# Kernel optimization log

Measured on AMD Instinct MI355X. Metric: run time of the kernel, lower is better.

Reference implementation:

```python
import jax, jax.numpy as jnp
import numpy as np

EPS = 1e-6  # VN-ReLU direction-norm epsilon
K_NN = 16


def vec_linear(x, W):
    # x: (B, Cin, 3, ...), W: (Cout, Cin) -> (B, Cout, 3, ...)
    return jnp.einsum('oi,bi...->bo...', W, x)


def vec_lna(x, W, U):
    # VecLinear + VN-LeakyReLU(negative_slope=0) acting on vector dim (axis 2)
    p = jnp.einsum('oi,bi...->bo...', W, x)   # feature map
    d = jnp.einsum('oi,bi...->bo...', U, x)   # direction map
    dot = jnp.sum(p * d, axis=2, keepdims=True)
    dsq = jnp.sum(d * d, axis=2, keepdims=True)
    return jnp.where(dot >= 0, p, p - (dot / (dsq + EPS)) * d)


def setup_inputs() -> dict:
    B, N = 2, 4096
    h, c, L = 128, 128, 4
    ks = jax.random.split(jax.random.key(0), 8)
    s = lambda k, shape, fan: (jax.random.normal(k, shape, jnp.float32) / np.sqrt(fan)).astype(jnp.float32)
    return {
        'x': jax.random.normal(ks[0], (B, 3, N), jnp.float32),
        'W_in': s(ks[1], (h, 3), 3),
        'U_in': s(ks[2], (h, 3), 3),
        'Wl': s(ks[3], (L, h, h), h),
        'Ul': s(ks[4], (L, h, h), h),
        'Wg': s(ks[5], (L, h, 2 * h), 2 * h),
        'Ug': s(ks[6], (L, h, 2 * h), 2 * h),
        'W_out': s(ks[7], (c, L * h), L * h),
    }


def reference(x, W_in, U_in, Wl, Ul, Wg, Ug, W_out):
    B, _, N = x.shape
    K = K_NN
    pts = jnp.transpose(x, (0, 2, 1))                      # (B, N, 3)
    # squared euclidean distance (same KNN ordering as torch.cdist p=2 + topk smallest)
    sq = jnp.sum(pts * pts, axis=-1)                       # (B, N)
    d2 = sq[:, :, None] + sq[:, None, :] - 2.0 * jnp.einsum('bnd,bmd->bnm', pts, pts)
    _, idx = jax.lax.top_k(-d2, K)                         # (B, N, K) nearest, sorted
    neighbors = jax.vmap(lambda p, i: p[i])(pts, idx)      # (B, N, K, 3) gather
    neighbors = jnp.transpose(neighbors, (0, 3, 1, 2))[:, None]  # (B, 1, 3, N, K)

    x4 = x[:, None]                                        # (B, 1, 3, N)
    x_pad = jnp.broadcast_to(x4[..., None], neighbors.shape)
    # F.normalize(x, dim=2) with eps=1e-12 clamp
    x_dir = x4 / jnp.maximum(jnp.linalg.norm(x4, axis=2, keepdims=True), 1e-12)
    cross = jnp.cross(jnp.broadcast_to(x_dir[..., None], neighbors.shape), neighbors, axis=2)
    y = jnp.concatenate([cross, neighbors - x_pad, x_pad], axis=1)  # (B, 3, 3, N, K)

    h_feat = vec_lna(y, W_in, U_in)                        # (B, h, 3, N, K)
    h_feat = jnp.mean(h_feat, axis=-1)                     # meanpool over K -> (B, h, 3, N)

    y = h_feat
    feats = []
    for i in range(Wl.shape[0]):
        y = vec_lna(y, Wl[i], Ul[i])                       # (B, h, 3, N)
        yg = jnp.mean(y, axis=-1, keepdims=True)
        y = jnp.concatenate([y, jnp.broadcast_to(yg, y.shape)], axis=1)  # (B, 2h, 3, N)
        y = vec_lna(y, Wg[i], Ug[i])                       # (B, h, 3, N)
        feats.append(y)

    out = vec_linear(jnp.concatenate(feats, axis=1), W_out)  # (B, c, 3, N)
    return (jnp.mean(out, axis=-1), out)
```

## Files before the change

### kernel.cpp

```cpp
#include <hip/hip_runtime.h>
#include <hip/hip_bf16.h>
#include <cfloat>


typedef __attribute__((ext_vector_type(8))) short short8;
typedef __attribute__((ext_vector_type(4))) float f32x4;

__device__ __forceinline__ unsigned short f2bf(float f) {
    union { float f; unsigned u; } v; v.f = f;
    unsigned r = v.u + 0x7fffu + ((v.u >> 16) & 1u);
    return (unsigned short)(r >> 16);
}
__device__ __forceinline__ float bf2f(unsigned short h) {
    union { unsigned u; float f; } v; v.u = ((unsigned)h) << 16;
    return v.f;
}

__global__ __launch_bounds__(256) void setup_kernel(const float* __restrict__ x,
                                                    float4* __restrict__ pts4,
                                                    const float* __restrict__ Wl,
                                                    const float* __restrict__ Ul,
                                                    const float* __restrict__ Wg,
                                                    const float* __restrict__ Ug,
                                                    const float* __restrict__ Wout,
                                                    unsigned short* __restrict__ Ah,
                                                    unsigned short* __restrict__ Al,
                                                    int N, int B) {
    int t = blockIdx.x * 256 + threadIdx.x;
    if (t < B * N) {
        int b = t / N, n = t - b * N;
        const float* xb = x + (long)b * 3 * N;
        float px = xb[n], py = xb[N + n], pz = xb[2 * N + n];
        pts4[t] = make_float4(px, py, pz, px * px + py * py + pz * pz);
    }
    int g, r, M; long base;
    if (t < 262144) { g = t >> 15; r = t & 32767; M = 256; base = (long)g << 15; }
    else { int t2 = t - 262144; g = 8 + (t2 >> 14); r = t2 & 16383; M = 128;
           base = 262144 + (long)(g - 8) * 16384; }
    int MF = M >> 4;
    int ks = r / (MF * 512);
    int mf = (r >> 9) % MF;
    int lane = (r >> 3) & 63;
    int j = r & 7;
    int m = mf * 16 + (lane & 15);
    int k = ks * 32 + ((lane >> 4) << 3) + j;
    const float* src; int ldw; int row;
    if (g < 4) {
        ldw = 128; row = m & 127;
        src = (m < 128) ? (Wl + (long)g * 128 * 128) : (Ul + (long)g * 128 * 128);
    } else if (g < 8) {
        ldw = 256; row = m & 127;
        int l = g - 4;
        src = (m < 128) ? (Wg + (long)l * 128 * 256) : (Ug + (long)l * 128 * 256);
    } else {
        ldw = 512; row = m;
        src = Wout + (g - 8) * 128;
    }
    float v = src[(long)row * ldw + k];
    unsigned short h = f2bf(v);
    Ah[base + r] = h;
    Al[base + r] = f2bf(v - bf2f(h));
}

__global__ __launch_bounds__(1024) void knn_kernel(const float4* __restrict__ pts4,
                                                   int* __restrict__ idxOut, int N) {
    __shared__ float4 cbuf[4096];
    int t = threadIdx.x;
    int tilesPerB = N / 16;
    int b = blockIdx.x / tilesPerB;
    int q = (blockIdx.x % tilesPerB) * 16 + (t >> 6);
    int lane = t & 63;

    for (int i = t; i < N; i += 1024) cbuf[i] = pts4[b * N + i];
    __syncthreads();

    float4 Q = cbuf[q];
    unsigned ku; int ki;

    {
        float4 C = cbuf[lane];
        float dot = Q.x * C.x + Q.y * C.y + Q.z * C.z;
        float d2 = Q.w + C.w - 2.0f * dot;
        unsigned u = __float_as_uint(d2);
        u ^= (unsigned)((int)u >> 31) | 0x80000000u;
        double key = (double)u * 4096.0 + (double)lane;
#pragma unroll
        for (int k = 2; k <= 64; k <<= 1) {
#pragma unroll
            for (int j = k >> 1; j > 0; j >>= 1) {
                double other = __shfl_xor(key, j);
                bool takeMin = (((lane & j) == 0) == ((lane & k) == 0));
                double mn = fmin(key, other), mx = fmax(key, other);
                key = takeMin ? mn : mx;
            }
        }
        long long kl = (long long)key;
        ki = (int)(kl & 4095);
        ku = (unsigned)(kl >> 12);
    }
    unsigned Tu = (unsigned)__builtin_amdgcn_readlane((int)ku, 15);

    for (int c0 = 64; c0 < N; c0 += 64) {
        float4 C = cbuf[c0 + lane];
        float dot = Q.x * C.x + Q.y * C.y + Q.z * C.z;
        float d2 = Q.w + C.w - 2.0f * dot;
        unsigned u = __float_as_uint(d2);
        u ^= (unsigned)((int)u >> 31) | 0x80000000u;
        int ci = c0 + lane;
        unsigned long long mask = __ballot(u <= Tu);
        while (mask) {
            int src = __ffsll(mask) - 1;
            mask &= mask - 1;
            unsigned vu = (unsigned)__builtin_amdgcn_readlane((int)u, src);
            int      vi = __builtin_amdgcn_readlane(ci, src);
            unsigned kum1 = (unsigned)__builtin_amdgcn_update_dpp(
                                (int)ku, (int)ku, 0x111, 0xF, 0xF, false);
            int      kim1 = __builtin_amdgcn_update_dpp(
                                ki, ki, 0x111, 0xF, 0xF, false);
            if (lane == 0) { kum1 = 0u; kim1 = (-2147483647 - 1); }
            bool lem1 = (vu < kum1) || (vu == kum1 && vi < kim1);
            bool ltj  = (vu < ku)   || (vu == ku   && vi < ki);
            unsigned knu = lem1 ? kum1 : (ltj ? vu : ku);
            int      kni = lem1 ? kim1 : (ltj ? vi : ki);
            if (lane < 16) { ku = knu; ki = kni; }
        }
        Tu = (unsigned)__builtin_amdgcn_readlane((int)ku, 15);
    }
    if (lane < 16) idxOut[(b * N + q) * 16 + lane] = ki;
}

__global__ __launch_bounds__(256) void edge_kernel(const float4* __restrict__ pts4,
                                                   const int* __restrict__ idx,
                                                   const float* __restrict__ Win,
                                                   const float* __restrict__ Uin,
                                                   unsigned short* __restrict__ Yh,
                                                   unsigned short* __restrict__ Yl,
                                                   int N) {
    __shared__ float4 nbuf[8][16];
    __shared__ float4 cpt[8];
    int nTiles = N / 8;
    int b = blockIdx.x / nTiles;
    int n0 = (blockIdx.x % nTiles) * 8;
    int t = threadIdx.x;
    if (t < 128) {
        int pl = t >> 4, k = t & 15;
        int nb = idx[(b * N + n0 + pl) * 16 + k];
        nbuf[pl][k] = pts4[b * N + nb];
    } else if (t < 136) {
        cpt[t - 128] = pts4[b * N + n0 + (t - 128)];
    }
    __syncthreads();
    int o = t & 127, h = t >> 7;
    float w0 = Win[o * 3], w1 = Win[o * 3 + 1], w2 = Win[o * 3 + 2];
    float u0 = Uin[o * 3], u1 = Uin[o * 3 + 1], u2 = Uin[o * 3 + 2];
    for (int pl = h * 4; pl < h * 4 + 4; ++pl) {
        float4 c4 = cpt[pl];
        float inv = 1.0f / fmaxf(sqrtf(c4.w), 1e-12f);
        float ax = c4.x * inv, ay = c4.y * inv, az = c4.z * inv;
        float a0 = 0.f, a1 = 0.f, a2 = 0.f;
        for (int k = 0; k < 16; ++k) {
            float4 nb = nbuf[pl][k];
            float cr0 = ay * nb.z - az * nb.y;
            float cr1 = az * nb.x - ax * nb.z;
            float cr2 = ax * nb.y - ay * nb.x;
            float df0 = nb.x - c4.x, df1 = nb.y - c4.y, df2 = nb.z - c4.z;
            float P0 = w0 * cr0 + w1 * df0 + w2 * c4.x;
            float P1 = w0 * cr1 + w1 * df1 + w2 * c4.y;
            float P2 = w0 * cr2 + w1 * df2 + w2 * c4.z;
            float D0 = u0 * cr0 + u1 * df0 + u2 * c4.x;
            float D1 = u0 * cr1 + u1 * df1 + u2 * c4.y;
            float D2 = u0 * cr2 + u1 * df2 + u2 * c4.z;
            float dot = P0 * D0 + P1 * D1 + P2 * D2;
            float dsq = D0 * D0 + D1 * D1 + D2 * D2;
            if (dot < 0.0f) {
                float s = dot / (dsq + 1e-6f);
                P0 -= s * D0; P1 -= s * D1; P2 -= s * D2;
            }
            a0 += P0; a1 += P1; a2 += P2;
        }
        float vals[3] = { a0 * (1.0f / 16.0f), a1 * (1.0f / 16.0f), a2 * (1.0f / 16.0f) };
        long n = n0 + pl;
#pragma unroll
        for (int c = 0; c < 3; ++c) {
            long off = ((long)(b * 3 + c) * 4096 + n) * 128 + o;
            unsigned short hh = f2bf(vals[c]);
            Yh[off] = hh;
            Yl[off] = f2bf(vals[c] - bf2f(hh));
        }
    }
}

__global__ __launch_bounds__(512, 1) void gemm0_kernel(
    const unsigned short* __restrict__ Aph, const unsigned short* __restrict__ Apl,
    long aOff,
    const unsigned short* __restrict__ Bh, const unsigned short* __restrict__ Bl,
    unsigned short* __restrict__ Oh, unsigned short* __restrict__ Ol,
    float* __restrict__ part)
{
    const int N = 4096;
    int t = threadIdx.x;
    int lane = t & 63, w = t >> 6;
    int mg = w >> 1, ng = w & 1;
    int b = blockIdx.x >> 7;
    int tile = blockIdx.x & 127;
    int ncol = tile * 32 + ng * 16 + (lane & 15);
    int kq = (lane >> 4) << 3;

    f32x4 accP[2][3] = {};
    f32x4 accD[2][3] = {};
    const unsigned short* AhB = Aph + aOff;
    const unsigned short* AlB = Apl + aOff;

#pragma unroll
    for (int ks = 0; ks < 4; ++ks) {
        short8 bh[3], bl[3];
#pragma unroll
        for (int c = 0; c < 3; ++c) {
            long boff = ((long)(b * 3 + c) * N + ncol) * 128 + ks * 32 + kq;
            bh[c] = *(const short8*)(Bh + boff);
            bl[c] = *(const short8*)(Bl + boff);
        }
#pragma unroll
        for (int pi = 0; pi < 2; ++pi) {
            int mf = 2 * mg + pi;
            long aoffP = (((long)ks * 16 + mf) * 64 + lane) * 8;
            short8 ahP = *(const short8*)(AhB + aoffP);
            short8 alP = *(const short8*)(AlB + aoffP);
#pragma unroll
            for (int c = 0; c < 3; ++c) {
                accP[pi][c] = __builtin_amdgcn_mfma_f32_16x16x32_bf16(ahP, bh[c], accP[pi][c], 0, 0, 0);
                accP[pi][c] = __builtin_amdgcn_mfma_f32_16x16x32_bf16(ahP, bl[c], accP[pi][c], 0, 0, 0);
                accP[pi][c] = __builtin_amdgcn_mfma_f32_16x16x32_bf16(alP, bh[c], accP[pi][c], 0, 0, 0);
            }
            long aoffD = (((long)ks * 16 + (8 + mf)) * 64 + lane) * 8;
            short8 ahD = *(const short8*)(AhB + aoffD);
            short8 alD = *(const short8*)(AlB + aoffD);
#pragma unroll
            for (int c = 0; c < 3; ++c) {
                accD[pi][c] = __builtin_amdgcn_mfma_f32_16x16x32_bf16(ahD, bh[c], accD[pi][c], 0, 0, 0);
                accD[pi][c] = __builtin_amdgcn_mfma_f32_16x16x32_bf16(ahD, bl[c], accD[pi][c], 0, 0, 0);
                accD[pi][c] = __builtin_amdgcn_mfma_f32_16x16x32_bf16(alD, bh[c], accD[pi][c], 0, 0, 0);
            }
        }
    }

#pragma unroll
    for (int pi = 0; pi < 2; ++pi) {
        int obase = 32 * mg + 16 * pi + ((lane >> 4) << 2);
        float Pv[3][4];
#pragma unroll
        for (int r = 0; r < 4; ++r) {
            float P[3], D[3];
#pragma unroll
            for (int c = 0; c < 3; ++c) { P[c] = accP[pi][c][r]; D[c] = accD[pi][c][r]; }
            float dot = P[0] * D[0] + P[1] * D[1] + P[2] * D[2];
            float dsq = D[0] * D[0] + D[1] * D[1] + D[2] * D[2];
            if (dot < 0.0f) {
                float s = dot / (dsq + 1e-6f);
                P[0] -= s * D[0]; P[1] -= s * D[1]; P[2] -= s * D[2];
            }
            Pv[0][r] = P[0]; Pv[1][r] = P[1]; Pv[2][r] = P[2];
        }
#pragma unroll
        for (int c = 0; c < 3; ++c) {
            unsigned short hs[4], ls[4];
#pragma unroll
            for (int r = 0; r < 4; ++r) {
                hs[r] = f2bf(Pv[c][r]);
                ls[r] = f2bf(Pv[c][r] - bf2f(hs[r]));
            }
            long ooff = ((long)(b * 3 + c) * N + ncol) * 128 + obase;
            *(ushort4*)(Oh + ooff) = make_ushort4(hs[0], hs[1], hs[2], hs[3]);
            *(ushort4*)(Ol + ooff) = make_ushort4(ls[0], ls[1], ls[2], ls[3]);
        }
#pragma unroll
        for (int c = 0; c < 3; ++c) {
#pragma unroll
            for (int r = 0; r < 4; ++r) {
                float v = Pv[c][r];
                v += __shfl_xor(v, 1);
                v += __shfl_xor(v, 2);
                v += __shfl_xor(v, 4);
                v += __shfl_xor(v, 8);
                if ((lane & 15) == 0)
                    part[((long)(b * 3 + c) * 256 + tile * 2 + ng) * 128 + (obase + r)] = v;
            }
        }
    }
}

template<bool HASNEXT>
__global__ __launch_bounds__(512, 1) void fused_kernel(
    const unsigned short* __restrict__ Aph, const unsigned short* __restrict__ Apl,
    long aOffG, long aOffOut, long aOffNext,
    unsigned short* __restrict__ y1h, unsigned short* __restrict__ y1l,
    const float* __restrict__ biasP, const float* __restrict__ biasD,
    float* __restrict__ Ofp, float* __restrict__ part, int accum)
{
    const int N = 4096;
    __shared__ unsigned short ylds[2][3][2][2048];
    int t = threadIdx.x;
    int lane = t & 63, w = t >> 6;
    int mg = w >> 1, ng = w & 1;
    int b = blockIdx.x >> 7;
    int tile = blockIdx.x & 127;
    int ncol = tile * 32 + ng * 16 + (lane & 15);
    int kq = (lane >> 4) << 3;

    {
        f32x4 accP[2][3] = {};
        f32x4 accD[2][3] = {};
        const unsigned short* AhB = Aph + aOffG;
        const unsigned short* AlB = Apl + aOffG;
#pragma unroll
        for (int ks = 0; ks < 4; ++ks) {
            short8 bh[3], bl[3];
#pragma unroll
            for (int c = 0; c < 3; ++c) {
                long boff = ((long)(b * 3 + c) * N + ncol) * 128 + ks * 32 + kq;
                bh[c] = *(const short8*)(y1h + boff);
                bl[c] = *(const short8*)(y1l + boff);
            }
#pragma unroll
            for (int pi = 0; pi < 2; ++pi) {
                int mf = 2 * mg + pi;
                long aoffP = (((long)ks * 16 + mf) * 64 + lane) * 8;
                short8 ahP = *(const short8*)(AhB + aoffP);
                short8 alP = *(const short8*)(AlB + aoffP);
#pragma unroll
                for (int c = 0; c < 3; ++c) {
                    accP[pi][c] = __builtin_amdgcn_mfma_f32_16x16x32_bf16(ahP, bh[c], accP[pi][c], 0, 0, 0);
                    accP[pi][c] = __builtin_amdgcn_mfma_f32_16x16x32_bf16(ahP, bl[c], accP[pi][c], 0, 0, 0);
                    accP[pi][c] = __builtin_amdgcn_mfma_f32_16x16x32_bf16(alP, bh[c], accP[pi][c], 0, 0, 0);
                }
                long aoffD = (((long)ks * 16 + (8 + mf)) * 64 + lane) * 8;
                short8 ahD = *(const short8*)(AhB + aoffD);
                short8 alD = *(const short8*)(AlB + aoffD);
#pragma unroll
                for (int c = 0; c < 3; ++c) {
                    accD[pi][c] = __builtin_amdgcn_mfma_f32_16x16x32_bf16(ahD, bh[c], accD[pi][c], 0, 0, 0);
                    accD[pi][c] = __builtin_amdgcn_mfma_f32_16x16x32_bf16(ahD, bl[c], accD[pi][c], 0, 0, 0);
                    accD[pi][c] = __builtin_amdgcn_mfma_f32_16x16x32_bf16(alD, bh[c], accD[pi][c], 0, 0, 0);
                }
            }
        }
#pragma unroll
        for (int pi = 0; pi < 2; ++pi) {
            int obase = 32 * mg + 16 * pi + ((lane >> 4) << 2);
            float Pv[3][4];
#pragma unroll
            for (int r = 0; r < 4; ++r) {
                int o = obase + r;
                float P[3], D[3];
#pragma unroll
                for (int c = 0; c < 3; ++c) {
                    long bb = ((long)(b * 128 + o)) * 3 + c;
                    P[c] = accP[pi][c][r] + biasP[bb];
                    D[c] = accD[pi][c][r] + biasD[bb];
                }
                float dot = P[0] * D[0] + P[1] * D[1] + P[2] * D[2];
                float dsq = D[0] * D[0] + D[1] * D[1] + D[2] * D[2];
                if (dot < 0.0f) {
                    float s = dot / (dsq + 1e-6f);
                    P[0] -= s * D[0]; P[1] -= s * D[1]; P[2] -= s * D[2];
                }
                Pv[0][r] = P[0]; Pv[1][r] = P[1]; Pv[2][r] = P[2];
            }
#pragma unroll
            for (int c = 0; c < 3; ++c) {
                unsigned short hs[4], ls[4];
#pragma unroll
                for (int r = 0; r < 4; ++r) {
                    hs[r] = f2bf(Pv[c][r]);
                    ls[r] = f2bf(Pv[c][r] - bf2f(hs[r]));
                }
                int li = ((obase >> 3) << 7) + ((lane & 15) << 3) + (obase & 7);
                *(ushort4*)&ylds[ng][c][0][li] = make_ushort4(hs[0], hs[1], hs[2], hs[3]);
                *(ushort4*)&ylds[ng][c][1][li] = make_ushort4(ls[0], ls[1], ls[2], ls[3]);
            }
        }
    }
    __syncthreads();

    {
        f32x4 accO[2][3] = {};
        const unsigned short* AoH = Aph + aOffOut;
        const unsigned short* AoL = Apl + aOffOut;
#pragma unroll
        for (int ks = 0; ks < 4; ++ks) {
            short8 yh[3], yl[3];
            int li = (((ks << 2) + (lane >> 4)) << 7) + ((lane & 15) << 3);
#pragma unroll
            for (int c = 0; c < 3; ++c) {
                yh[c] = *(const short8*)&ylds[ng][c][0][li];
                yl[c] = *(const short8*)&ylds[ng][c][1][li];
            }
#pragma unroll
            for (int pi = 0; pi < 2; ++pi) {
                int mf = 2 * mg + pi;
                long aoff = (((long)ks * 8 + mf) * 64 + lane) * 8;
                short8 ah = *(const short8*)(AoH + aoff);
                short8 al = *(const short8*)(AoL + aoff);
#pragma unroll
                for (int c = 0; c < 3; ++c) {
                    accO[pi][c] = __builtin_amdgcn_mfma_f32_16x16x32_bf16(ah, yh[c], accO[pi][c], 0, 0, 0);
                    accO[pi][c] = __builtin_amdgcn_mfma_f32_16x16x32_bf16(ah, yl[c], accO[pi][c], 0, 0, 0);
                    accO[pi][c] = __builtin_amdgcn_mfma_f32_16x16x32_bf16(al, yh[c], accO[pi][c], 0, 0, 0);
                }
            }
        }
#pragma unroll
        for (int pi = 0; pi < 2; ++pi) {
            int obase = 32 * mg + 16 * pi + ((lane >> 4) << 2);
#pragma unroll
            for (int r = 0; r < 4; ++r) {
                int o = obase + r;
#pragma unroll
                for (int c = 0; c < 3; ++c) {
                    long off = ((long)(b * 128 + o) * 3 + c) * N + ncol;
                    float v = accO[pi][c][r];
                    if (accum) v += Ofp[off];
                    Ofp[off] = v;
                }
            }
        }
    }

    if (HASNEXT) {
        f32x4 accP[2][3] = {};
        f32x4 accD[2][3] = {};
        const unsigned short* AnH = Aph + aOffNext;
        const unsigned short* AnL = Apl + aOffNext;
#pragma unroll
        for (int ks = 0; ks < 4; ++ks) {
            short8 bh[3], bl[3];
            int li = (((ks << 2) + (lane >> 4)) << 7) + ((lane & 15) << 3);
#pragma unroll
            for (int c = 0; c < 3; ++c) {
                bh[c] = *(const short8*)&ylds[ng][c][0][li];
                bl[c] = *(const short8*)&ylds[ng][c][1][li];
            }
#pragma unroll
            for (int pi = 0; pi < 2; ++pi) {
                int mf = 2 * mg + pi;
                long aoffP = (((long)ks * 16 + mf) * 64 + lane) * 8;
                short8 ahP = *(const short8*)(AnH + aoffP);
                short8 alP = *(const short8*)(AnL + aoffP);
#pragma unroll
                for (int c = 0; c < 3; ++c) {
                    accP[pi][c] = __builtin_amdgcn_mfma_f32_16x16x32_bf16(ahP, bh[c], accP[pi][c], 0, 0, 0);
                    accP[pi][c] = __builtin_amdgcn_mfma_f32_16x16x32_bf16(ahP, bl[c], accP[pi][c], 0, 0, 0);
                    accP[pi][c] = __builtin_amdgcn_mfma_f32_16x16x32_bf16(alP, bh[c], accP[pi][c], 0, 0, 0);
                }
                long aoffD = (((long)ks * 16 + (8 + mf)) * 64 + lane) * 8;
                short8 ahD = *(const short8*)(AnH + aoffD);
                short8 alD = *(const short8*)(AnL + aoffD);
#pragma unroll
                for (int c = 0; c < 3; ++c) {
                    accD[pi][c] = __builtin_amdgcn_mfma_f32_16x16x32_bf16(ahD, bh[c], accD[pi][c], 0, 0, 0);
                    accD[pi][c] = __builtin_amdgcn_mfma_f32_16x16x32_bf16(ahD, bl[c], accD[pi][c], 0, 0, 0);
                    accD[pi][c] = __builtin_amdgcn_mfma_f32_16x16x32_bf16(alD, bh[c], accD[pi][c], 0, 0, 0);
                }
            }
        }
#pragma unroll
        for (int pi = 0; pi < 2; ++pi) {
            int obase = 32 * mg + 16 * pi + ((lane >> 4) << 2);
            float Pv[3][4];
#pragma unroll
            for (int r = 0; r < 4; ++r) {
                float P[3], D[3];
#pragma unroll
                for (int c = 0; c < 3; ++c) { P[c] = accP[pi][c][r]; D[c] = accD[pi][c][r]; }
                float dot = P[0] * D[0] + P[1] * D[1] + P[2] * D[2];
                float dsq = D[0] * D[0] + D[1] * D[1] + D[2] * D[2];
                if (dot < 0.0f) {
                    float s = dot / (dsq + 1e-6f);
                    P[0] -= s * D[0]; P[1] -= s * D[1]; P[2] -= s * D[2];
                }
                Pv[0][r] = P[0]; Pv[1][r] = P[1]; Pv[2][r] = P[2];
            }
#pragma unroll
            for (int c = 0; c < 3; ++c) {
                unsigned short hs[4], ls[4];
#pragma unroll
                for (int r = 0; r < 4; ++r) {
                    hs[r] = f2bf(Pv[c][r]);
                    ls[r] = f2bf(Pv[c][r] - bf2f(hs[r]));
                }
                long ooff = ((long)(b * 3 + c) * N + ncol) * 128 + obase;
                *(ushort4*)(y1h + ooff) = make_ushort4(hs[0], hs[1], hs[2], hs[3]);
                *(ushort4*)(y1l + ooff) = make_ushort4(ls[0], ls[1], ls[2], ls[3]);
            }
#pragma unroll
            for (int c = 0; c < 3; ++c) {
#pragma unroll
                for (int r = 0; r < 4; ++r) {
                    float v = Pv[c][r];
                    v += __shfl_xor(v, 1);
                    v += __shfl_xor(v, 2);
                    v += __shfl_xor(v, 4);
                    v += __shfl_xor(v, 8);
                    if ((lane & 15) == 0)
                        part[((long)(b * 3 + c) * 256 + tile * 2 + ng) * 128 + (obase + r)] = v;
                }
            }
        }
    }
}

__global__ __launch_bounds__(1024) void ygredbias_kernel(const float* __restrict__ part,
                                                         const float* __restrict__ Wg,
                                                         const float* __restrict__ Ug,
                                                         float* __restrict__ biasP,
                                                         float* __restrict__ biasD) {
    __shared__ float red[8][128];
    __shared__ float ygs[128];
    int bc = blockIdx.x;
    int t = threadIdx.x;
    int o = t & 127, g = t >> 7;
    float s = 0.f;
    for (int seg = g * 32; seg < g * 32 + 32; ++seg)
        s += part[((long)bc * 256 + seg) * 128 + o];
    red[g][o] = s;
    __syncthreads();
    if (t < 128) {
        float r = 0.f;
#pragma unroll
        for (int k = 0; k < 8; ++k) r += red[k][t];
        ygs[t] = r * (1.0f / 4096.0f);
    }
    __syncthreads();
    if (t < 256) {
        int oo = t & 127; bool isD = t >= 128;
        const float* row = (isD ? Ug : Wg) + oo * 256 + 128;
        float s2 = 0.f;
        for (int i = 0; i < 128; ++i) s2 = fmaf(row[i], ygs[i], s2);
        int b = bc / 3, c = bc % 3;
        (isD ? biasD : biasP)[((long)(b * 128 + oo)) * 3 + c] = s2;
    }
}

__global__ __launch_bounds__(256) void reduce_mean_kernel(const float* __restrict__ src, long bs,
                                                          float* __restrict__ dst, int N) {
    __shared__ float red[256];
    int row = blockIdx.x;
    int b = row / 384; int rr = row % 384;
    const float* p = src + (long)b * bs + (long)rr * N;
    float s = 0.f;
    for (int i = threadIdx.x; i < N; i += 256) s += p[i];
    red[threadIdx.x] = s;
    __syncthreads();
    for (int st = 128; st > 0; st >>= 1) {
        if (threadIdx.x < st) red[threadIdx.x] += red[threadIdx.x + st];
        __syncthreads();
    }
    if (threadIdx.x == 0) dst[row] = red[0] / (float)N;
}

extern "C" void kernel_launch(void* const* d_in, const int* in_sizes, int n_in,
                              void* d_out, int out_size, void* d_ws, size_t ws_size,
                              hipStream_t stream) {
    const float* x    = (const float*)d_in[0];
    const float* Win  = (const float*)d_in[1];
    const float* Uin  = (const float*)d_in[2];
    const float* Wl   = (const float*)d_in[3];
    const float* Ul   = (const float*)d_in[4];
    const float* Wg   = (const float*)d_in[5];
    const float* Ug   = (const float*)d_in[6];
    const float* Wout = (const float*)d_in[7];

    const int B = 2, N = 4096, H = 128;
    float* out0 = (float*)d_out;
    float* out1 = out0 + (long)B * H * 3;

    float* ws = (float*)d_ws;
    long off = 0;
    float4* pts4 = (float4*)ws;                  off += (long)B * N * 4;
    int* idx = (int*)(ws + off);                 off += (long)B * N * 16;
    const long ACT = (long)B * 3 * N * H;
    unsigned short* f0h = (unsigned short*)(ws + off);  off += ACT / 2;
    unsigned short* f0l = (unsigned short*)(ws + off);  off += ACT / 2;
    unsigned short* y1h = (unsigned short*)(ws + off);  off += ACT / 2;
    unsigned short* y1l = (unsigned short*)(ws + off);  off += ACT / 2;
    unsigned short* Aph = (unsigned short*)(ws + off);  off += 327680 / 2;
    unsigned short* Apl = (unsigned short*)(ws + off);  off += 327680 / 2;
    float* part  = ws + off;                     off += 6L * 256 * 128;
    float* biasP = ws + off;                     off += B * H * 3;
    float* biasD = ws + off;                     off += B * H * 3;

    long bs128 = (long)H * 3 * N;

    setup_kernel<<<1280, 256, 0, stream>>>(x, pts4, Wl, Ul, Wg, Ug, Wout, Aph, Apl, N, B);
    knn_kernel<<<B * (N / 16), 1024, 0, stream>>>(pts4, idx, N);
    edge_kernel<<<B * (N / 8), 256, 0, stream>>>(pts4, idx, Win, Uin, f0h, f0l, N);

    gemm0_kernel<<<256, 512, 0, stream>>>(Aph, Apl, 0L, f0h, f0l, y1h, y1l, part);

    for (int l = 0; l < 4; ++l) {
        ygredbias_kernel<<<6, 1024, 0, stream>>>(part,
            Wg + (long)l * H * 256, Ug + (long)l * H * 256, biasP, biasD);
        long aG = (long)(4 + l) * 32768;
        long aO = 262144 + (long)l * 16384;
        if (l < 3) {
            fused_kernel<true><<<256, 512, 0, stream>>>(
                Aph, Apl, aG, aO, (long)(l + 1) * 32768,
                y1h, y1l, biasP, biasD, out1, part, l > 0 ? 1 : 0);
        } else {
            fused_kernel<false><<<256, 512, 0, stream>>>(
                Aph, Apl, aG, aO, 0L,
                y1h, y1l, biasP, biasD, out1, part, 1);
        }
    }
    reduce_mean_kernel<<<B * H * 3, 256, 0, stream>>>(out1, bs128, out0, N);
}
```

Measured before the change: 254.2 us.

## Fuse edge feature computation into first GEMM and compute output means from partials

The edge (neighbor feature + VN-ReLU + meanpool) stage now runs inside the first GEMM kernel. Each 512-thread block computes its 32 points' features straight into shared memory in the MFMA operand layout, so the bf16 hi/lo activation buffer is never written to or read back from global memory. The final fused layer also writes per-tile column partial sums, and a small reduction kernel over those partials replaces the full-read mean over the output. In exchange, the edge compute now runs on only 256 blocks with lower parallelism, and shared memory use rises.

```diff
diff --git a/kernel.cpp b/kernel.cpp
--- a/kernel.cpp
+++ b/kernel.cpp
@@ -129,103 +129,90 @@
     if (lane < 16) idxOut[(b * N + q) * 16 + lane] = ki;
 }
 
-__global__ __launch_bounds__(256) void edge_kernel(const float4* __restrict__ pts4,
-                                                   const int* __restrict__ idx,
-                                                   const float* __restrict__ Win,
-                                                   const float* __restrict__ Uin,
-                                                   unsigned short* __restrict__ Yh,
-                                                   unsigned short* __restrict__ Yl,
-                                                   int N) {
-    __shared__ float4 nbuf[8][16];
-    __shared__ float4 cpt[8];
-    int nTiles = N / 8;
-    int b = blockIdx.x / nTiles;
-    int n0 = (blockIdx.x % nTiles) * 8;
-    int t = threadIdx.x;
-    if (t < 128) {
-        int pl = t >> 4, k = t & 15;
-        int nb = idx[(b * N + n0 + pl) * 16 + k];
-        nbuf[pl][k] = pts4[b * N + nb];
-    } else if (t < 136) {
-        cpt[t - 128] = pts4[b * N + n0 + (t - 128)];
-    }
-    __syncthreads();
-    int o = t & 127, h = t >> 7;
-    float w0 = Win[o * 3], w1 = Win[o * 3 + 1], w2 = Win[o * 3 + 2];
-    float u0 = Uin[o * 3], u1 = Uin[o * 3 + 1], u2 = Uin[o * 3 + 2];
-    for (int pl = h * 4; pl < h * 4 + 4; ++pl) {
-        float4 c4 = cpt[pl];
-        float inv = 1.0f / fmaxf(sqrtf(c4.w), 1e-12f);
-        float ax = c4.x * inv, ay = c4.y * inv, az = c4.z * inv;
-        float a0 = 0.f, a1 = 0.f, a2 = 0.f;
-        for (int k = 0; k < 16; ++k) {
-            float4 nb = nbuf[pl][k];
-            float cr0 = ay * nb.z - az * nb.y;
-            float cr1 = az * nb.x - ax * nb.z;
-            float cr2 = ax * nb.y - ay * nb.x;
-            float df0 = nb.x - c4.x, df1 = nb.y - c4.y, df2 = nb.z - c4.z;
-            float P0 = w0 * cr0 + w1 * df0 + w2 * c4.x;
-            float P1 = w0 * cr1 + w1 * df1 + w2 * c4.y;
-            float P2 = w0 * cr2 + w1 * df2 + w2 * c4.z;
-            float D0 = u0 * cr0 + u1 * df0 + u2 * c4.x;
-            float D1 = u0 * cr1 + u1 * df1 + u2 * c4.y;
-            float D2 = u0 * cr2 + u1 * df2 + u2 * c4.z;
-            float dot = P0 * D0 + P1 * D1 + P2 * D2;
-            float dsq = D0 * D0 + D1 * D1 + D2 * D2;
-            if (dot < 0.0f) {
-                float s = dot / (dsq + 1e-6f);
-                P0 -= s * D0; P1 -= s * D1; P2 -= s * D2;
-            }
-            a0 += P0; a1 += P1; a2 += P2;
-        }
-        float vals[3] = { a0 * (1.0f / 16.0f), a1 * (1.0f / 16.0f), a2 * (1.0f / 16.0f) };
-        long n = n0 + pl;
-#pragma unroll
-        for (int c = 0; c < 3; ++c) {
-            long off = ((long)(b * 3 + c) * 4096 + n) * 128 + o;
-            unsigned short hh = f2bf(vals[c]);
-            Yh[off] = hh;
-            Yl[off] = f2bf(vals[c] - bf2f(hh));
-        }
-    }
-}
-
-__global__ __launch_bounds__(512, 1) void gemm0_kernel(
+__global__ __launch_bounds__(512, 1) void edgegemm0_kernel(
+    const float4* __restrict__ pts4, const int* __restrict__ idx,
+    const float* __restrict__ Win, const float* __restrict__ Uin,
     const unsigned short* __restrict__ Aph, const unsigned short* __restrict__ Apl,
-    long aOff,
-    const unsigned short* __restrict__ Bh, const unsigned short* __restrict__ Bl,
     unsigned short* __restrict__ Oh, unsigned short* __restrict__ Ol,
-    float* __restrict__ part)
+    float* __restrict__ part, int N)
 {
-    const int N = 4096;
+    __shared__ float4 nbuf[32][16];
+    __shared__ float4 cpt[32];
+    __shared__ unsigned short flds[2][3][2][2048];
     int t = threadIdx.x;
     int lane = t & 63, w = t >> 6;
     int mg = w >> 1, ng = w & 1;
     int b = blockIdx.x >> 7;
     int tile = blockIdx.x & 127;
+    int n0 = tile * 32;
+
+    {
+        int pl = t >> 4, k = t & 15;
+        int nb = idx[(b * N + n0 + pl) * 16 + k];
+        nbuf[pl][k] = pts4[b * N + nb];
+        if (t < 32) cpt[t] = pts4[b * N + n0 + t];
+    }
+    __syncthreads();
+    {
+        int o = t & 127, grp = t >> 7;
+        float w0 = Win[o * 3], w1 = Win[o * 3 + 1], w2 = Win[o * 3 + 2];
+        float u0 = Uin[o * 3], u1 = Uin[o * 3 + 1], u2 = Uin[o * 3 + 2];
+        for (int pl = grp * 8; pl < grp * 8 + 8; ++pl) {
+            float4 c4 = cpt[pl];
+            float inv = 1.0f / fmaxf(sqrtf(c4.w), 1e-12f);
+            float ax = c4.x * inv, ay = c4.y * inv, az = c4.z * inv;
+            float a0 = 0.f, a1 = 0.f, a2 = 0.f;
+            for (int k = 0; k < 16; ++k) {
+                float4 nb = nbuf[pl][k];
+                float cr0 = ay * nb.z - az * nb.y;
+                float cr1 = az * nb.x - ax * nb.z;
+                float cr2 = ax * nb.y - ay * nb.x;
+                float df0 = nb.x - c4.x, df1 = nb.y - c4.y, df2 = nb.z - c4.z;
+                float P0 = w0 * cr0 + w1 * df0 + w2 * c4.x;
+                float P1 = w0 * cr1 + w1 * df1 + w2 * c4.y;
+                float P2 = w0 * cr2 + w1 * df2 + w2 * c4.z;
+                float D0 = u0 * cr0 + u1 * df0 + u2 * c4.x;
+                float D1 = u0 * cr1 + u1 * df1 + u2 * c4.y;
+                float D2 = u0 * cr2 + u1 * df2 + u2 * c4.z;
+                float dot = P0 * D0 + P1 * D1 + P2 * D2;
+                float dsq = D0 * D0 + D1 * D1 + D2 * D2;
+                if (dot < 0.0f) {
+                    float s = dot / (dsq + 1e-6f);
+                    P0 -= s * D0; P1 -= s * D1; P2 -= s * D2;
+                }
+                a0 += P0; a1 += P1; a2 += P2;
+            }
+            float vals[3] = { a0 * (1.0f / 16.0f), a1 * (1.0f / 16.0f), a2 * (1.0f / 16.0f) };
+            int ngg = pl >> 4, col = pl & 15;
+            int li = ((o >> 3) << 7) + (col << 3) + (o & 7);
+#pragma unroll
+            for (int c = 0; c < 3; ++c) {
+                unsigned short hh = f2bf(vals[c]);
+                flds[ngg][c][0][li] = hh;
+                flds[ngg][c][1][li] = f2bf(vals[c] - bf2f(hh));
+            }
+        }
+    }
+    __syncthreads();
+
     int ncol = tile * 32 + ng * 16 + (lane & 15);
-    int kq = (lane >> 4) << 3;
-
     f32x4 accP[2][3] = {};
     f32x4 accD[2][3] = {};
-    const unsigned short* AhB = Aph + aOff;
-    const unsigned short* AlB = Apl + aOff;
-
 #pragma unroll
     for (int ks = 0; ks < 4; ++ks) {
         short8 bh[3], bl[3];
+        int li = (((ks << 2) + (lane >> 4)) << 7) + ((lane & 15) << 3);
 #pragma unroll
         for (int c = 0; c < 3; ++c) {
-            long boff = ((long)(b * 3 + c) * N + ncol) * 128 + ks * 32 + kq;
-            bh[c] = *(const short8*)(Bh + boff);
-            bl[c] = *(const short8*)(Bl + boff);
+            bh[c] = *(const short8*)&flds[ng][c][0][li];
+            bl[c] = *(const short8*)&flds[ng][c][1][li];
         }
 #pragma unroll
         for (int pi = 0; pi < 2; ++pi) {
             int mf = 2 * mg + pi;
             long aoffP = (((long)ks * 16 + mf) * 64 + lane) * 8;
-            short8 ahP = *(const short8*)(AhB + aoffP);
-            short8 alP = *(const short8*)(AlB + aoffP);
+            short8 ahP = *(const short8*)(Aph + aoffP);
+            short8 alP = *(const short8*)(Apl + aoffP);
 #pragma unroll
             for (int c = 0; c < 3; ++c) {
                 accP[pi][c] = __builtin_amdgcn_mfma_f32_16x16x32_bf16(ahP, bh[c], accP[pi][c], 0, 0, 0);
@@ -233,8 +220,8 @@
                 accP[pi][c] = __builtin_amdgcn_mfma_f32_16x16x32_bf16(alP, bh[c], accP[pi][c], 0, 0, 0);
             }
             long aoffD = (((long)ks * 16 + (8 + mf)) * 64 + lane) * 8;
-            short8 ahD = *(const short8*)(AhB + aoffD);
-            short8 alD = *(const short8*)(AlB + aoffD);
+            short8 ahD = *(const short8*)(Aph + aoffD);
+            short8 alD = *(const short8*)(Apl + aoffD);
 #pragma unroll
             for (int c = 0; c < 3; ++c) {
                 accD[pi][c] = __builtin_amdgcn_mfma_f32_16x16x32_bf16(ahD, bh[c], accD[pi][c], 0, 0, 0);
@@ -412,6 +399,7 @@
 #pragma unroll
         for (int pi = 0; pi < 2; ++pi) {
             int obase = 32 * mg + 16 * pi + ((lane >> 4) << 2);
+            float Ov[3][4];
 #pragma unroll
             for (int r = 0; r < 4; ++r) {
                 int o = obase + r;
@@ -421,6 +409,22 @@
                     float v = accO[pi][c][r];
                     if (accum) v += Ofp[off];
                     Ofp[off] = v;
+                    Ov[c][r] = v;
+                }
+            }
+            if (!HASNEXT) {
+#pragma unroll
+                for (int c = 0; c < 3; ++c) {
+#pragma unroll
+                    for (int r = 0; r < 4; ++r) {
+                        float v = Ov[c][r];
+                        v += __shfl_xor(v, 1);
+                        v += __shfl_xor(v, 2);
+                        v += __shfl_xor(v, 4);
+                        v += __shfl_xor(v, 8);
+                        if ((lane & 15) == 0)
+                            part[((long)(b * 3 + c) * 256 + tile * 2 + ng) * 128 + (obase + r)] = v;
+                    }
                 }
             }
         }
@@ -541,21 +545,24 @@
     }
 }
 
-__global__ __launch_bounds__(256) void reduce_mean_kernel(const float* __restrict__ src, long bs,
-                                                          float* __restrict__ dst, int N) {
-    __shared__ float red[256];
-    int row = blockIdx.x;
-    int b = row / 384; int rr = row % 384;
-    const float* p = src + (long)b * bs + (long)rr * N;
+__global__ __launch_bounds__(1024) void out0red_kernel(const float* __restrict__ part,
+                                                       float* __restrict__ out0) {
+    __shared__ float red[8][128];
+    int bc = blockIdx.x;
+    int t = threadIdx.x;
+    int o = t & 127, g = t >> 7;
     float s = 0.f;
-    for (int i = threadIdx.x; i < N; i += 256) s += p[i];
-    red[threadIdx.x] = s;
+    for (int seg = g * 32; seg < g * 32 + 32; ++seg)
+        s += part[((long)bc * 256 + seg) * 128 + o];
+    red[g][o] = s;
     __syncthreads();
-    for (int st = 128; st > 0; st >>= 1) {
-        if (threadIdx.x < st) red[threadIdx.x] += red[threadIdx.x + st];
-        __syncthreads();
-    }
-    if (threadIdx.x == 0) dst[row] = red[0] / (float)N;
+    if (t < 128) {
+        float r = 0.f;
+#pragma unroll
+        for (int k = 0; k < 8; ++k) r += red[k][t];
+        int b = bc / 3, c = bc % 3;
+        out0[((long)(b * 128) + t) * 3 + c] = r * (1.0f / 4096.0f);
+    }
 }
 
 extern "C" void kernel_launch(void* const* d_in, const int* in_sizes, int n_in,
@@ -579,8 +586,6 @@
     float4* pts4 = (float4*)ws;                  off += (long)B * N * 4;
     int* idx = (int*)(ws + off);                 off += (long)B * N * 16;
     const long ACT = (long)B * 3 * N * H;
-    unsigned short* f0h = (unsigned short*)(ws + off);  off += ACT / 2;
-    unsigned short* f0l = (unsigned short*)(ws + off);  off += ACT / 2;
     unsigned short* y1h = (unsigned short*)(ws + off);  off += ACT / 2;
     unsigned short* y1l = (unsigned short*)(ws + off);  off += ACT / 2;
     unsigned short* Aph = (unsigned short*)(ws + off);  off += 327680 / 2;
@@ -589,13 +594,11 @@
     float* biasP = ws + off;                     off += B * H * 3;
     float* biasD = ws + off;                     off += B * H * 3;
 
-    long bs128 = (long)H * 3 * N;
-
     setup_kernel<<<1280, 256, 0, stream>>>(x, pts4, Wl, Ul, Wg, Ug, Wout, Aph, Apl, N, B);
     knn_kernel<<<B * (N / 16), 1024, 0, stream>>>(pts4, idx, N);
-    edge_kernel<<<B * (N / 8), 256, 0, stream>>>(pts4, idx, Win, Uin, f0h, f0l, N);
-
-    gemm0_kernel<<<256, 512, 0, stream>>>(Aph, Apl, 0L, f0h, f0l, y1h, y1l, part);
+
+    edgegemm0_kernel<<<256, 512, 0, stream>>>(pts4, idx, Win, Uin,
+                                              Aph, Apl, y1h, y1l, part, N);
 
     for (int l = 0; l < 4; ++l) {
         ygredbias_kernel<<<6, 1024, 0, stream>>>(part,
@@ -612,5 +615,5 @@
                 y1h, y1l, biasP, biasD, out1, part, 1);
         }
     }
-    reduce_mean_kernel<<<B * H * 3, 256, 0, stream>>>(out1, bs128, out0, N);
-}
+    out0red_kernel<<<6, 1024, 0, stream>>>(part, out0);
+}
```

Result: no change. 250.6 us (-1.4%).
